# Optimization experiments

Measured on AMD Instinct MI355X. Metric: run time of the kernel, lower is better.

Reference implementation:

```python
import jax, jax.numpy as jnp
import numpy as np

D_MODEL = 768
D_STATE = 16
B, L = 4, 2048


def setup_inputs() -> dict:
    key = jax.random.key(0)
    ks = jax.random.split(key, 8)
    s = 1.0 / np.sqrt(D_MODEL)
    x = jax.random.normal(ks[0], (B, L, D_MODEL), jnp.float32)
    W_in = jax.random.normal(ks[1], (D_MODEL, 2 * D_MODEL), jnp.float32) * s
    b_in = jnp.zeros((2 * D_MODEL,), jnp.float32)
    W_B = jax.random.normal(ks[2], (D_MODEL, D_STATE), jnp.float32) * s
    b_B = jnp.zeros((D_STATE,), jnp.float32)
    W_C = jax.random.normal(ks[3], (D_MODEL, D_STATE), jnp.float32) * s
    b_C = jnp.zeros((D_STATE,), jnp.float32)
    W_delta = jax.random.normal(ks[4], (D_MODEL, D_MODEL), jnp.float32) * s
    b_delta = jnp.zeros((D_MODEL,), jnp.float32)
    W_out = jax.random.normal(ks[5], (D_MODEL, D_MODEL), jnp.float32) * s
    b_out = jnp.zeros((D_MODEL,), jnp.float32)
    # A_log init from the module: log(A + 1) with A[s, d] = s+1
    A_log = jnp.log(jnp.arange(1, D_STATE + 1, dtype=jnp.float32)[:, None]
                    * jnp.ones((1, D_MODEL), jnp.float32) + 1.0)
    D = jnp.ones((D_MODEL,), jnp.float32)
    return {"x": x, "W_in": W_in, "b_in": b_in, "W_B": W_B, "b_B": b_B,
            "W_C": W_C, "b_C": b_C, "W_delta": W_delta, "b_delta": b_delta,
            "W_out": W_out, "b_out": b_out, "A_log": A_log, "D": D}


def reference(x, W_in, b_in, W_B, b_B, W_C, b_C, W_delta, b_delta,
              W_out, b_out, A_log, D):
    x_proj = x @ W_in + b_in                      # (B, L, 2*d_model)
    x_main, x_gate = jnp.split(x_proj, 2, axis=-1)
    x_main = jax.nn.silu(x_main)
    B_mat = x_main @ W_B + b_B                    # (B, L, d_state)
    C_mat = x_main @ W_C + b_C                    # (B, L, d_state)
    delta = jax.nn.softplus(x_main @ W_delta + b_delta) + 0.0001
    delta = jnp.clip(delta, 0.0001, 1.0)          # (B, L, d_model)
    A = jnp.clip(-jnp.exp(A_log), -5.0, -0.1)     # (d_state, d_model)
    deltaA = jnp.exp(jnp.clip(delta[:, :, None, :] * A[None, None, :, :], -2.0, 0.0))
    deltaA = jnp.clip(deltaA, 0.05, 1.0)          # (B, L, d_state, d_model)
    deltaB_u = jnp.clip(delta[:, :, None, :] * B_mat[:, :, :, None] * x_main[:, :, None, :],
                        -5.0, 5.0)                # (B, L, d_state, d_model)

    def binary_operator(elem1, elem2):
        A1, Bu1 = elem1
        A2, Bu2 = elem2
        A_c = jnp.clip(A2 * A1, 1e-06, 10.0)
        Bu_c = jnp.clip(A2 * Bu1 + Bu2, -100.0, 100.0)
        return (A_c, Bu_c)

    # elementwise combine => scanning along axis=1 of the batched arrays is
    # identical to vmapping a per-batch scan over axis 0
    _, h_Bu = jax.lax.associative_scan(binary_operator, (deltaA, deltaB_u), axis=1)
    y = jnp.einsum('blsd,bls->bld', h_Bu, C_mat)
    y = jnp.clip(y, -10.0, 10.0)
    y = y + x_main * D[None, None, :]
    y = y * jax.nn.silu(x_gate)
    y = jnp.clip(y @ W_out + b_out, -10.0, 10.0)
    return y
```

## Files before the change

kernel.cpp:

```cpp
#include <hip/hip_runtime.h>
#include <hip/hip_bf16.h>
#include <cstdint>
#include <cstddef>

#define D_MODEL 768
#define D_STATE 16
#define BB      4
#define LL      2048
#define M_TOT   (BB*LL)
#define NCHUNK  64
#define LCH     (LL/NCHUNK)
#define N_DBC   896
#define KC      768
#define NTK     (KC/32)

typedef __attribute__((ext_vector_type(8))) short bf16x8;
typedef __attribute__((ext_vector_type(4))) float f32x4;

__device__ __forceinline__ float clampf_(float x, float lo, float hi) {
    return fminf(fmaxf(x, lo), hi);
}
__device__ __forceinline__ float siluf_(float x) {
    return x / (1.f + __expf(-x));
}
__device__ __forceinline__ unsigned short f2bf(float f) {
    unsigned u = __float_as_uint(f);
    u += 0x7fffu + ((u >> 16) & 1u);
    return (unsigned short)(u >> 16);
}
__device__ __forceinline__ float bf2f(unsigned short u) {
    return __uint_as_float(((unsigned)u) << 16);
}
__device__ __forceinline__ void gload16(void* lds, const void* g) {
    __builtin_amdgcn_global_load_lds(
        (const __attribute__((address_space(1))) void*)g,
        (__attribute__((address_space(3))) void*)lds, 16, 0, 0);
}


__global__ __launch_bounds__(256) void k_convert_x(const float* __restrict__ x,
                                                   unsigned short* __restrict__ xb, int n4) {
    int i = blockIdx.x * 256 + threadIdx.x;
    if (i >= n4) return;
    float4 v = ((const float4*)x)[i];
    ushort4 o;
    o.x = f2bf(v.x); o.y = f2bf(v.y); o.z = f2bf(v.z); o.w = f2bf(v.w);
    ((ushort4*)xb)[i] = o;
}

__global__ __launch_bounds__(256) void k_prep_A(const float* __restrict__ A_log,
                                                float* __restrict__ A_cl, int n) {
    int i = blockIdx.x * 256 + threadIdx.x;
    if (i < n) A_cl[i] = clampf_(-__expf(A_log[i]), -5.f, -0.1f);
}

__global__ __launch_bounds__(256) void k_transpose_bf16(const float* __restrict__ src,
                                                        unsigned short* __restrict__ dst,
                                                        int R, int C) {
    __shared__ float tile[32][33];
    int tx = threadIdx.x & 31, ty = threadIdx.x >> 5;
    int c0 = blockIdx.x * 32, r0 = blockIdx.y * 32;
    #pragma unroll
    for (int rr = ty; rr < 32; rr += 8)
        tile[rr][tx] = src[(size_t)(r0 + rr) * C + c0 + tx];
    __syncthreads();
    #pragma unroll
    for (int rr = ty; rr < 32; rr += 8)
        dst[(size_t)(c0 + rr) * R + r0 + tx] = f2bf(tile[tx][rr]);
}

__global__ __launch_bounds__(256) void k_fill_bc(const float* __restrict__ W_B,
                                                 const float* __restrict__ W_C,
                                                 unsigned short* __restrict__ WdBC) {
    int idx = blockIdx.x * 256 + threadIdx.x;
    if (idx >= 128 * D_MODEL) return;
    int r = idx / D_MODEL + D_MODEL, k = idx % D_MODEL;
    unsigned short v = 0;
    if (r < D_MODEL + 16)       v = f2bf(W_B[k * 16 + (r - D_MODEL)]);
    else if (r < D_MODEL + 32)  v = f2bf(W_C[k * 16 + (r - D_MODEL - 16)]);
    WdBC[(size_t)r * D_MODEL + k] = v;
}

__global__ __launch_bounds__(256) void k_bias_dbc(const float* __restrict__ b_delta,
                                                  const float* __restrict__ b_B,
                                                  const float* __restrict__ b_C,
                                                  float* __restrict__ bias) {
    int i = blockIdx.x * 256 + threadIdx.x;
    if (i >= N_DBC) return;
    float v = 0.f;
    if (i < D_MODEL)            v = b_delta[i];
    else if (i < D_MODEL + 16)  v = b_B[i - D_MODEL];
    else if (i < D_MODEL + 32)  v = b_C[i - D_MODEL - 16];
    bias[i] = v;
}

template<int EPI>
__global__ __launch_bounds__(512) void k_gemm(const unsigned short* __restrict__ A,
                                              const unsigned short* __restrict__ Bt,
                                              const float* __restrict__ bias,
                                              int gx,
                                              float* __restrict__ out_f,
                                              float* __restrict__ out_f2,
                                              unsigned short* __restrict__ out_b0,
                                              unsigned short* __restrict__ out_b1) {
    __shared__ __align__(16) unsigned short As0[256 * 32], As1[256 * 32], As2[256 * 32];
    __shared__ __align__(16) unsigned short Bs0[128 * 32], Bs1[128 * 32], Bs2[128 * 32];
    const int tid = threadIdx.x;
    const int wave = tid >> 6, lane = tid & 63;
    const int wm = wave >> 1, wn = wave & 1;

    const int nwg = gridDim.x;
    const int wg = blockIdx.x;
    int swz = wg;
    if ((nwg & 7) == 0) {
        const int q = nwg >> 3;
        swz = (wg & 7) * q + (wg >> 3);
    }
    const int bx = swz % gx, by = swz / gx;
    const int m0 = by * 256, n0 = bx * 128;
    const int lr = lane & 15;

    const int jg = ((tid & 3) ^ ((tid >> 3) & 3));
    const unsigned short* gA0 = &A [(size_t)(m0 +       (tid >> 2)) * KC + jg * 8];
    const unsigned short* gA1 = &A [(size_t)(m0 + 128 + (tid >> 2)) * KC + jg * 8];
    const unsigned short* gB0 = &Bt[(size_t)(n0 +       (tid >> 2)) * KC + jg * 8];
    const int ldsA0 = (wave * 64) * 8;
    const int ldsA1 = (512 + wave * 64) * 8;
    const int ldsB0 = (wave * 64) * 8;

    const int swzk = (((lane >> 4) ^ (lane >> 1)) & 3) * 8;

    f32x4 acc[4][4] = {};

    auto stageT = [&](unsigned short* Ab, unsigned short* Bb, int kt) {
        gload16(&Ab[ldsA0], gA0 + kt);
        gload16(&Ab[ldsA1], gA1 + kt);
        gload16(&Bb[ldsB0], gB0 + kt);
    };
    auto computeT = [&](const unsigned short* Ab, const unsigned short* Bb) {
        bf16x8 af[4], bfr[4];
        #pragma unroll
        for (int mt = 0; mt < 4; ++mt)
            af[mt] = *(const bf16x8*)&Ab[(wm * 64 + mt * 16 + lr) * 32 + swzk];
        #pragma unroll
        for (int nt = 0; nt < 4; ++nt)
            bfr[nt] = *(const bf16x8*)&Bb[(wn * 64 + nt * 16 + lr) * 32 + swzk];
        #pragma unroll
        for (int mt = 0; mt < 4; ++mt)
            #pragma unroll
            for (int nt = 0; nt < 4; ++nt)
                acc[mt][nt] = __builtin_amdgcn_mfma_f32_16x16x32_bf16(
                    af[mt], bfr[nt], acc[mt][nt], 0, 0, 0);
    };

    stageT(As0, Bs0, 0);
    stageT(As1, Bs1, 32);
    stageT(As2, Bs2, 64);
    asm volatile("s_waitcnt vmcnt(6)" ::: "memory");
    __builtin_amdgcn_sched_barrier(0);
    __builtin_amdgcn_s_barrier();

#define SUBSTEP(Ab, Bb, t) do {                                   \
        computeT(Ab, Bb);                                         \
        asm volatile("s_waitcnt lgkmcnt(0)" ::: "memory");        \
        __builtin_amdgcn_sched_barrier(0);                        \
        __builtin_amdgcn_s_barrier();                             \
        stageT(Ab, Bb, ((t) + 3) << 5);                           \
        asm volatile("s_waitcnt vmcnt(6)" ::: "memory");          \
        __builtin_amdgcn_sched_barrier(0);                        \
        __builtin_amdgcn_s_barrier();                             \
    } while (0)

    for (int t = 0; t < NTK - 3; t += 3) {
        SUBSTEP(As0, Bs0, t);
        SUBSTEP(As1, Bs1, t + 1);
        SUBSTEP(As2, Bs2, t + 2);
    }
#undef SUBSTEP
    computeT(As0, Bs0);
    asm volatile("s_waitcnt vmcnt(3)" ::: "memory");
    __builtin_amdgcn_sched_barrier(0);
    __builtin_amdgcn_s_barrier();
    computeT(As1, Bs1);
    asm volatile("s_waitcnt vmcnt(0)" ::: "memory");
    __builtin_amdgcn_sched_barrier(0);
    __builtin_amdgcn_s_barrier();
    computeT(As2, Bs2);

    #pragma unroll
    for (int mt = 0; mt < 4; ++mt) {
        int row = m0 + wm * 64 + mt * 16 + (lane >> 4) * 4;
        #pragma unroll
        for (int nt = 0; nt < 4; ++nt) {
            int col = n0 + wn * 64 + nt * 16 + (lane & 15);
            #pragma unroll
            for (int i = 0; i < 4; ++i) {
                int r = row + i;
                float v = acc[mt][nt][i] + bias[col];
                if (EPI == 0) {
                    float s = siluf_(v);
                    if (col < D_MODEL) out_b0[(size_t)r * D_MODEL + col] = f2bf(s);
                    else               out_b1[(size_t)r * D_MODEL + (col - D_MODEL)] = f2bf(s);
                } else if (EPI == 1) {
                    if (col < D_MODEL) {
                        float sp = (v > 20.f) ? v : log1pf(__expf(v));
                        out_b0[(size_t)r * D_MODEL + col] = f2bf(clampf_(sp + 1e-4f, 1e-4f, 1.f));
                    } else if (col < D_MODEL + 16) {
                        out_f[(size_t)r * D_STATE + (col - D_MODEL)] = v;
                    } else if (col < D_MODEL + 32) {
                        out_f2[(size_t)r * D_STATE + (col - D_MODEL - 16)] = v;
                    }
                } else {
                    out_f[(size_t)r * D_MODEL + col] = clampf_(v, -10.f, 10.f);
                }
            }
        }
    }
}

__global__ __launch_bounds__(256) void k_scanA(const unsigned short* __restrict__ dlt,
                                               const unsigned short* __restrict__ xm,
                                               const float* __restrict__ Bm,
                                               const float* __restrict__ A_cl,
                                               float* __restrict__ h_end,
                                               float* __restrict__ Aprod) {
    const int d = blockIdx.x * 256 + threadIdx.x;
    const int c = blockIdx.y, b = blockIdx.z;
    __shared__ float Bsh[LCH][D_STATE];
    const int rowbase = b * LL + c * LCH;
    for (int i = threadIdx.x; i < LCH * D_STATE; i += 256)
        ((float*)Bsh)[i] = Bm[(size_t)rowbase * D_STATE + i];
    __syncthreads();

    float Asv[16], h[16], ap[16];
    #pragma unroll
    for (int s = 0; s < 16; ++s) {
        Asv[s] = A_cl[s * D_MODEL + d];
        h[s] = 0.f; ap[s] = 1.f;
    }
    for (int tt = 0; tt < LCH; ++tt) {
        const size_t rowoff = (size_t)(rowbase + tt);
        float dltv = bf2f(dlt[rowoff * D_MODEL + d]);
        float xv   = bf2f(xm [rowoff * D_MODEL + d]);
        float dx = dltv * xv;
        #pragma unroll
        for (int s = 0; s < 16; ++s) {
            float dA  = __expf(fmaxf(dltv * Asv[s], -2.f));
            float dBu = clampf_(dx * Bsh[tt][s], -5.f, 5.f);
            h[s] = clampf_(fmaf(dA, h[s], dBu), -100.f, 100.f);
            ap[s] *= dA;
        }
    }
    const size_t off = (((size_t)b * NCHUNK + c) * D_STATE) * D_MODEL + d;
    #pragma unroll
    for (int s = 0; s < 16; ++s) {
        h_end[off + (size_t)s * D_MODEL] = h[s];
        Aprod[off + (size_t)s * D_MODEL] = ap[s];
    }
}

__global__ __launch_bounds__(256) void k_scanB(const float* __restrict__ h_end,
                                               const float* __restrict__ Aprod,
                                               float* __restrict__ h_in) {
    const int idx = blockIdx.x * 256 + threadIdx.x;
    const int d = idx % D_MODEL;
    const int rest = idx / D_MODEL;
    const int s = rest & 15, b = rest >> 4;
    float hc = 0.f;
    for (int c = 0; c < NCHUNK; ++c) {
        const size_t off = (((size_t)b * NCHUNK + c) * D_STATE + s) * D_MODEL + d;
        h_in[off] = hc;
        hc = Aprod[off] * hc + h_end[off];
    }
}

__global__ __launch_bounds__(256) void k_scanC(const unsigned short* __restrict__ dlt,
                                               const unsigned short* __restrict__ xm,
                                               const float* __restrict__ Bm,
                                               const float* __restrict__ Cm,
                                               const float* __restrict__ A_cl,
                                               const float* __restrict__ h_in,
                                               const float* __restrict__ Dvec,
                                               const unsigned short* __restrict__ gate,
                                               unsigned short* __restrict__ ymid) {
    const int d = blockIdx.x * 256 + threadIdx.x;
    const int c = blockIdx.y, b = blockIdx.z;
    __shared__ float Bsh[LCH][D_STATE];
    __shared__ float Csh[LCH][D_STATE];
    const int rowbase = b * LL + c * LCH;
    for (int i = threadIdx.x; i < LCH * D_STATE; i += 256) {
        ((float*)Bsh)[i] = Bm[(size_t)rowbase * D_STATE + i];
        ((float*)Csh)[i] = Cm[(size_t)rowbase * D_STATE + i];
    }
    __syncthreads();

    float Asv[16], h[16];
    const size_t coff = (((size_t)b * NCHUNK + c) * D_STATE) * D_MODEL + d;
    #pragma unroll
    for (int s = 0; s < 16; ++s) {
        Asv[s] = A_cl[s * D_MODEL + d];
        h[s] = h_in[coff + (size_t)s * D_MODEL];
    }
    const float Dv = Dvec[d];
    for (int tt = 0; tt < LCH; ++tt) {
        const size_t rowoff = (size_t)(rowbase + tt);
        float dltv = bf2f(dlt[rowoff * D_MODEL + d]);
        float xv   = bf2f(xm [rowoff * D_MODEL + d]);
        float dx = dltv * xv;
        float y = 0.f;
        #pragma unroll
        for (int s = 0; s < 16; ++s) {
            float dA  = __expf(fmaxf(dltv * Asv[s], -2.f));
            float dBu = clampf_(dx * Bsh[tt][s], -5.f, 5.f);
            h[s] = clampf_(fmaf(dA, h[s], dBu), -100.f, 100.f);
            y = fmaf(h[s], Csh[tt][s], y);
        }
        y = clampf_(y, -10.f, 10.f);
        y = fmaf(xv, Dv, y);
        y *= bf2f(gate[rowoff * D_MODEL + d]);
        ymid[rowoff * D_MODEL + d] = f2bf(y);
    }
}

extern "C" void kernel_launch(void* const* d_in, const int* in_sizes, int n_in,
                              void* d_out, int out_size, void* d_ws, size_t ws_size,
                              hipStream_t stream) {
    const float* x       = (const float*)d_in[0];
    const float* W_in    = (const float*)d_in[1];
    const float* b_in    = (const float*)d_in[2];
    const float* W_B     = (const float*)d_in[3];
    const float* b_B     = (const float*)d_in[4];
    const float* W_C     = (const float*)d_in[5];
    const float* b_C     = (const float*)d_in[6];
    const float* W_delta = (const float*)d_in[7];
    const float* b_delta = (const float*)d_in[8];
    const float* W_out   = (const float*)d_in[9];
    const float* b_out   = (const float*)d_in[10];
    const float* A_log   = (const float*)d_in[11];
    const float* Dvec    = (const float*)d_in[12];
    float* out = (float*)d_out;

    char* p = (char*)d_ws;
    auto alloc = [&](size_t bytes) {
        char* r = p;
        p += (bytes + 255) & ~(size_t)255;
        return r;
    };
    unsigned short* xb    = (unsigned short*)alloc((size_t)M_TOT * D_MODEL * 2);
    unsigned short* Wint  = (unsigned short*)alloc((size_t)2 * D_MODEL * D_MODEL * 2);
    unsigned short* WdBC  = (unsigned short*)alloc((size_t)N_DBC * D_MODEL * 2);
    unsigned short* Wot   = (unsigned short*)alloc((size_t)D_MODEL * D_MODEL * 2);
    float*          bdbc  = (float*)alloc((size_t)N_DBC * 4);
    unsigned short* xm_b  = (unsigned short*)alloc((size_t)M_TOT * D_MODEL * 2);
    unsigned short* gate_b= (unsigned short*)alloc((size_t)M_TOT * D_MODEL * 2);
    unsigned short* dlt_b = (unsigned short*)alloc((size_t)M_TOT * D_MODEL * 2);
    float*          Bm    = (float*)alloc((size_t)M_TOT * D_STATE * 4);
    float*          Cm    = (float*)alloc((size_t)M_TOT * D_STATE * 4);
    float*          A_cl  = (float*)alloc((size_t)D_STATE * D_MODEL * 4);
    float*          h_end = (float*)alloc((size_t)BB * NCHUNK * D_STATE * D_MODEL * 4);
    float*          Aprod = (float*)alloc((size_t)BB * NCHUNK * D_STATE * D_MODEL * 4);
    float*          h_in  = (float*)alloc((size_t)BB * NCHUNK * D_STATE * D_MODEL * 4);
    unsigned short* ymid  = (unsigned short*)alloc((size_t)M_TOT * D_MODEL * 2);

    k_convert_x<<<(M_TOT * D_MODEL / 4 + 255) / 256, 256, 0, stream>>>(x, xb, M_TOT * D_MODEL / 4);
    k_prep_A<<<(D_STATE * D_MODEL + 255) / 256, 256, 0, stream>>>(A_log, A_cl, D_STATE * D_MODEL);
    k_transpose_bf16<<<dim3(2 * D_MODEL / 32, D_MODEL / 32), 256, 0, stream>>>(W_in, Wint, D_MODEL, 2 * D_MODEL);
    k_transpose_bf16<<<dim3(D_MODEL / 32, D_MODEL / 32), 256, 0, stream>>>(W_delta, WdBC, D_MODEL, D_MODEL);
    k_fill_bc<<<(128 * D_MODEL + 255) / 256, 256, 0, stream>>>(W_B, W_C, WdBC);
    k_bias_dbc<<<(N_DBC + 255) / 256, 256, 0, stream>>>(b_delta, b_B, b_C, bdbc);
    k_transpose_bf16<<<dim3(D_MODEL / 32, D_MODEL / 32), 256, 0, stream>>>(W_out, Wot, D_MODEL, D_MODEL);

    k_gemm<0><<<dim3((2 * D_MODEL / 128) * (M_TOT / 256)), 512, 0, stream>>>(
        xb, Wint, b_in, 2 * D_MODEL / 128, nullptr, nullptr, xm_b, gate_b);
    k_gemm<1><<<dim3((N_DBC / 128) * (M_TOT / 256)), 512, 0, stream>>>(
        xm_b, WdBC, bdbc, N_DBC / 128, Bm, Cm, dlt_b, nullptr);
    k_scanA<<<dim3(D_MODEL / 256, NCHUNK, BB), 256, 0, stream>>>(dlt_b, xm_b, Bm, A_cl, h_end, Aprod);
    k_scanB<<<(BB * D_STATE * D_MODEL) / 256, 256, 0, stream>>>(h_end, Aprod, h_in);
    k_scanC<<<dim3(D_MODEL / 256, NCHUNK, BB), 256, 0, stream>>>(
        dlt_b, xm_b, Bm, Cm, A_cl, h_in, Dvec, gate_b, ymid);
    k_gemm<2><<<dim3((D_MODEL / 128) * (M_TOT / 256)), 512, 0, stream>>>(
        ymid, Wot, b_out, D_MODEL / 128, out, nullptr, nullptr, nullptr);
}
```

Measured before the change: 207.0 us.

## Replace direct-to-LDS triple buffering with register-staged double buffering in GEMM

The GEMM main loop no longer uses global_load_lds into three LDS stages. It now loads the next tile into registers before the MFMA compute and writes it to LDS with a row-based XOR swizzle after a single barrier, using two LDS buffers. This cuts LDS use from three stages to two, which could allow more resident workgroups, and removes one barrier per k-step. In exchange it adds VGPR pressure and VALU/LDS-write instructions, and the prefetch distance shrinks.

Result: no change. 203.1 us (-1.9%).

```diff
diff --git a/kernel.cpp b/kernel.cpp
--- a/kernel.cpp
+++ b/kernel.cpp
@@ -30,11 +30,6 @@
 }
 __device__ __forceinline__ float bf2f(unsigned short u) {
     return __uint_as_float(((unsigned)u) << 16);
-}
-__device__ __forceinline__ void gload16(void* lds, const void* g) {
-    __builtin_amdgcn_global_load_lds(
-        (const __attribute__((address_space(1))) void*)g,
-        (__attribute__((address_space(3))) void*)lds, 16, 0, 0);
 }
 
 
@@ -103,8 +98,8 @@
                                               float* __restrict__ out_f2,
                                               unsigned short* __restrict__ out_b0,
                                               unsigned short* __restrict__ out_b1) {
-    __shared__ __align__(16) unsigned short As0[256 * 32], As1[256 * 32], As2[256 * 32];
-    __shared__ __align__(16) unsigned short Bs0[128 * 32], Bs1[128 * 32], Bs2[128 * 32];
+    __shared__ __align__(16) unsigned short As0[256 * 32], As1[256 * 32];
+    __shared__ __align__(16) unsigned short Bs0[128 * 32], Bs1[128 * 32];
     const int tid = threadIdx.x;
     const int wave = tid >> 6, lane = tid & 63;
     const int wm = wave >> 1, wn = wave & 1;
@@ -120,22 +115,29 @@
     const int m0 = by * 256, n0 = bx * 128;
     const int lr = lane & 15;
 
-    const int jg = ((tid & 3) ^ ((tid >> 3) & 3));
-    const unsigned short* gA0 = &A [(size_t)(m0 +       (tid >> 2)) * KC + jg * 8];
-    const unsigned short* gA1 = &A [(size_t)(m0 + 128 + (tid >> 2)) * KC + jg * 8];
-    const unsigned short* gB0 = &Bt[(size_t)(n0 +       (tid >> 2)) * KC + jg * 8];
-    const int ldsA0 = (wave * 64) * 8;
-    const int ldsA1 = (512 + wave * 64) * 8;
-    const int ldsB0 = (wave * 64) * 8;
+    const int row0 = tid >> 2, jl = tid & 3;
+    const int jj = jl ^ ((row0 >> 1) & 3);
+    const unsigned short* gA0 = &A [(size_t)(m0 +       row0) * KC + jl * 8];
+    const unsigned short* gA1 = &A [(size_t)(m0 + 128 + row0) * KC + jl * 8];
+    const unsigned short* gB0 = &Bt[(size_t)(n0 +       row0) * KC + jl * 8];
+    const int wA0 = (row0 * 4 + jj) * 8;
+    const int wA1 = ((row0 + 128) * 4 + jj) * 8;
+    const int wB0 = (row0 * 4 + jj) * 8;
 
     const int swzk = (((lane >> 4) ^ (lane >> 1)) & 3) * 8;
 
     f32x4 acc[4][4] = {};
-
-    auto stageT = [&](unsigned short* Ab, unsigned short* Bb, int kt) {
-        gload16(&Ab[ldsA0], gA0 + kt);
-        gload16(&Ab[ldsA1], gA1 + kt);
-        gload16(&Bb[ldsB0], gB0 + kt);
+    float4 ra0, ra1, rb0;
+
+    auto loadT = [&](int kt) {
+        ra0 = *(const float4*)(gA0 + kt);
+        ra1 = *(const float4*)(gA1 + kt);
+        rb0 = *(const float4*)(gB0 + kt);
+    };
+    auto writeT = [&](unsigned short* Ab, unsigned short* Bb) {
+        *(float4*)&Ab[wA0] = ra0;
+        *(float4*)&Ab[wA1] = ra1;
+        *(float4*)&Bb[wB0] = rb0;
     };
     auto computeT = [&](const unsigned short* Ab, const unsigned short* Bb) {
         bf16x8 af[4], bfr[4];
@@ -153,39 +155,30 @@
                     af[mt], bfr[nt], acc[mt][nt], 0, 0, 0);
     };
 
-    stageT(As0, Bs0, 0);
-    stageT(As1, Bs1, 32);
-    stageT(As2, Bs2, 64);
-    asm volatile("s_waitcnt vmcnt(6)" ::: "memory");
+    loadT(0);
+    writeT(As0, Bs0);
+    loadT(32);
+    writeT(As1, Bs1);
+    asm volatile("s_waitcnt lgkmcnt(0)" ::: "memory");
     __builtin_amdgcn_sched_barrier(0);
     __builtin_amdgcn_s_barrier();
+    __builtin_amdgcn_sched_barrier(0);
 
 #define SUBSTEP(Ab, Bb, t) do {                                   \
+        if ((t) + 2 < NTK) loadT(((t) + 2) << 5);                 \
         computeT(Ab, Bb);                                         \
         asm volatile("s_waitcnt lgkmcnt(0)" ::: "memory");        \
         __builtin_amdgcn_sched_barrier(0);                        \
         __builtin_amdgcn_s_barrier();                             \
-        stageT(Ab, Bb, ((t) + 3) << 5);                           \
-        asm volatile("s_waitcnt vmcnt(6)" ::: "memory");          \
         __builtin_amdgcn_sched_barrier(0);                        \
-        __builtin_amdgcn_s_barrier();                             \
+        if ((t) + 2 < NTK) writeT(Ab, Bb);                        \
     } while (0)
 
-    for (int t = 0; t < NTK - 3; t += 3) {
+    for (int t = 0; t < NTK; t += 2) {
         SUBSTEP(As0, Bs0, t);
         SUBSTEP(As1, Bs1, t + 1);
-        SUBSTEP(As2, Bs2, t + 2);
     }
 #undef SUBSTEP
-    computeT(As0, Bs0);
-    asm volatile("s_waitcnt vmcnt(3)" ::: "memory");
-    __builtin_amdgcn_sched_barrier(0);
-    __builtin_amdgcn_s_barrier();
-    computeT(As1, Bs1);
-    asm volatile("s_waitcnt vmcnt(0)" ::: "memory");
-    __builtin_amdgcn_sched_barrier(0);
-    __builtin_amdgcn_s_barrier();
-    computeT(As2, Bs2);
 
     #pragma unroll
     for (int mt = 0; mt < 4; ++mt) {
```
